# Kernel optimization log

Hardware: AMD Instinct MI355X
Metric: run time of the kernel (lower is better)

Reference implementation:

```python
import jax, jax.numpy as jnp
import numpy as np
import math

# ---- static config (matches init_kwargs) ----
N_USERS = 40000
N_ITEMS = 30000
N_ENTITIES = 80000
N_REL = 8            # edge_type in [1, N_REL), relation_emb has N_REL-1 rows
DIM = 64
N_HEADS = 2
D_K = DIM // N_HEADS
N_HOPS = 2
E_KG = 800000
E_UI = 600000


def setup_inputs() -> dict:
    key = jax.random.key(0)
    ks = jax.random.split(key, 10)
    return {
        "user_emb": jax.random.normal(ks[0], (N_USERS, DIM), jnp.float32) * 0.1,
        "entity_emb": jax.random.normal(ks[1], (N_ENTITIES, DIM), jnp.float32) * 0.1,
        "relation_emb": jax.random.normal(ks[2], (N_REL - 1, DIM), jnp.float32) * 0.1,
        "W_Q": jax.random.normal(ks[3], (DIM, DIM), jnp.float32) * (1.0 / math.sqrt(DIM)),
        "inter_edge_w": jax.random.uniform(ks[4], (E_UI,), jnp.float32),
        "edge_head": jax.random.randint(ks[5], (E_KG,), 0, N_ENTITIES, jnp.int32),
        "edge_tail": jax.random.randint(ks[6], (E_KG,), 0, N_ENTITIES, jnp.int32),
        "edge_type": jax.random.randint(ks[7], (E_KG,), 1, N_REL, jnp.int32),
        "inter_user": jax.random.randint(ks[8], (E_UI,), 0, N_USERS, jnp.int32),
        "inter_item": jax.random.randint(ks[9], (E_UI,), 0, N_ENTITIES, jnp.int32),
    }


def _seg_softmax(x, seg, n):
    """Numerically-stable softmax over edges grouped by segment id (scatter_softmax)."""
    m = jax.ops.segment_max(x, seg, num_segments=n)
    m = jnp.where(jnp.isneginf(m), 0.0, m)          # empty segments
    ex = jnp.exp(x - m[seg])
    s = jax.ops.segment_sum(ex, seg, num_segments=n)
    return ex / (s[seg] + 1e-16)


def _edge_attn(entity_emb, relation_emb, W_Q, head, tail, etype):
    """Per-edge multi-head attention logits: q_h . (k_h * rel_h) / sqrt(d_k). [E, H]"""
    q = (entity_emb[head] @ W_Q).reshape(-1, N_HEADS, D_K)
    k = (entity_emb[tail] @ W_Q).reshape(-1, N_HEADS, D_K)
    k = k * relation_emb[etype - 1].reshape(-1, N_HEADS, D_K)
    return (q * k).sum(-1) * (1.0 / math.sqrt(D_K))


def _l2norm(x):
    return x / jnp.maximum(jnp.linalg.norm(x, axis=-1, keepdims=True), 1e-12)


def reference(user_emb, entity_emb, relation_emb, W_Q, inter_edge_w,
              edge_head, edge_tail, edge_type, inter_user, inter_item):
    # ---- norm_attn_computer (logits detached in original torch code) ----
    logits = jax.lax.stop_gradient(
        _edge_attn(entity_emb, relation_emb, W_Q, edge_head, edge_tail, edge_type).mean(-1))  # [E]
    score = _seg_softmax(logits, edge_head, N_ENTITIES)
    deg = jax.ops.segment_sum(jnp.ones((E_KG,), jnp.float32), edge_head, num_segments=N_ENTITIES)
    edge_attn_score = score * deg[edge_head]                                   # [E]
    item_attn_sumed = (jax.ops.segment_sum(logits, edge_head, num_segments=N_ENTITIES)
                       + jax.ops.segment_sum(logits, edge_tail, num_segments=N_ENTITIES))[:N_ITEMS]

    # ---- HGT message passing hops (mess_dropout=False) ----
    e, u = entity_emb, user_emb
    e_res, u_res = entity_emb, user_emb
    for _ in range(N_HOPS):
        attn = _edge_attn(e, relation_emb, W_Q, edge_head, edge_tail, edge_type)  # [E, H]
        s = _seg_softmax(attn, edge_head, N_ENTITIES)                              # [E, H]
        neigh = (e[edge_tail] * relation_emb[edge_type - 1]).reshape(-1, N_HEADS, D_K) * s[..., None]
        e_agg = jax.ops.segment_sum(neigh.reshape(-1, DIM), edge_head, num_segments=N_ENTITIES)
        # bipartite user<->item aggregation with interaction weights
        u_agg = jax.ops.segment_sum(inter_edge_w[:, None] * e[inter_item], inter_user,
                                    num_segments=N_USERS)
        e_agg = e_agg + jax.ops.segment_sum(inter_edge_w[:, None] * u[inter_user], inter_item,
                                            num_segments=N_ENTITIES)
        e, u = _l2norm(e_agg), _l2norm(u_agg)
        e_res, u_res = e_res + e, u_res + u

    node_res_emb = jnp.concatenate([u_res, e_res], axis=0)   # [N_USERS+N_ENTITIES, DIM]
    return node_res_emb, edge_attn_score, item_attn_sumed
```

## Files before the change

kernel.cpp:

```cpp
#include <hip/hip_runtime.h>
#include <math.h>

#define NUSERS 40000
#define NENT   80000
#define NITEMS 30000
#define DIM    64
#define EKG    800000
#define EUI    600000
#define NTOT   (NENT + NUSERS + NENT)
#define UBASE  NENT
#define IBASE  (NENT + NUSERS)

struct __align__(8) us4 { unsigned short x, y, z, w; };
static __device__ __forceinline__ float b2f(unsigned short b) {
    return __uint_as_float(((unsigned)b) << 16);
}
static __device__ __forceinline__ unsigned short f2b(float f) {
    unsigned u = __float_as_uint(f);
    return (unsigned short)((u + 0x7FFFu + ((u >> 16) & 1u)) >> 16);
}
static __device__ __forceinline__ float4 us4tof(us4 v) {
    return make_float4(b2f(v.x), b2f(v.y), b2f(v.z), b2f(v.w));
}
static __device__ __forceinline__ float4 ld4b(const unsigned short* p) {
    return us4tof(*(const us4*)p);
}
static __device__ __forceinline__ void st4b(unsigned short* p, float a, float b, float c, float d) {
    us4 v = {f2b(a), f2b(b), f2b(c), f2b(d)};
    *(us4*)p = v;
}

static __device__ __forceinline__ float grp16_sum(float v) {
    v += __shfl_xor(v, 1);
    v += __shfl_xor(v, 2);
    v += __shfl_xor(v, 4);
    v += __shfl_xor(v, 8);
    return v;
}

__global__ void count_kernel(const int* __restrict__ ehead, const int* __restrict__ etail,
                             const int* __restrict__ etype,
                             const int* __restrict__ iuser, const int* __restrict__ iitem,
                             const float* __restrict__ user_emb,
                             int* __restrict__ cnt,
                             int* __restrict__ hrK, int* __restrict__ hrU, int* __restrict__ hrI,
                             int* __restrict__ tpack, unsigned short* __restrict__ u0b) {
    int e = blockIdx.x * blockDim.x + threadIdx.x;
    if (e < EKG) {
        int h = __builtin_nontemporal_load(&ehead[e]);
        int r = atomicAdd(&cnt[h], 1);
        hrK[e] = (h << 15) | r;
        tpack[e] = __builtin_nontemporal_load(&etail[e]) |
                   ((__builtin_nontemporal_load(&etype[e]) - 1) << 20);
    }
    if (e < EUI) {
        int u = __builtin_nontemporal_load(&iuser[e]);
        int r = atomicAdd(&cnt[UBASE + u], 1);
        hrU[e] = (u << 16) | r;
        int it = __builtin_nontemporal_load(&iitem[e]);
        int r2 = atomicAdd(&cnt[IBASE + it], 1);
        hrI[e] = (it << 15) | r2;
    }
    if (e < NUSERS * (DIM / 4)) {
        float4 vv = *(const float4*)(user_emb + (size_t)e * 4);
        st4b(u0b + (size_t)e * 4, vv.x, vv.y, vv.z, vv.w);
    }
}

#define SCHUNK 2048
#define SBLOCKS ((NTOT + SCHUNK - 1) / SCHUNK)

__global__ void scanA_kernel(const int* __restrict__ cnt, int* __restrict__ bsum) {
    int b = blockIdx.x, tid = threadIdx.x;
    int base = b * SCHUNK + tid * 8;
    int ts = 0;
#pragma unroll
    for (int k = 0; k < 8; k++) {
        int i = base + k;
        ts += (i < NTOT) ? cnt[i] : 0;
    }
#pragma unroll
    for (int d = 1; d < 64; d <<= 1) ts += __shfl_xor(ts, d);
    __shared__ int ws[4];
    if ((tid & 63) == 0) ws[tid >> 6] = ts;
    __syncthreads();
    if (tid == 0) bsum[b] = ws[0] + ws[1] + ws[2] + ws[3];
}

__global__ void scanB_kernel(const int* __restrict__ bsum, int* __restrict__ bpre,
                             int* __restrict__ off) {
    int lane = threadIdx.x;
    int carry = 0;
    for (int base = 0; base < SBLOCKS; base += 64) {
        int i = base + lane;
        int x = (i < SBLOCKS) ? bsum[i] : 0;
        int inc = x;
#pragma unroll
        for (int d = 1; d < 64; d <<= 1) {
            int t = __shfl_up(inc, d);
            if (lane >= d) inc += t;
        }
        if (i < SBLOCKS) bpre[i] = carry + inc - x;
        carry += __shfl(inc, 63);
    }
    if (lane == 0) off[NTOT] = carry;
}

__global__ void scanC_kernel(const int* __restrict__ cnt, const int* __restrict__ bpre,
                             int* __restrict__ off) {
    __shared__ int wtot[4];
    int b = blockIdx.x, tid = threadIdx.x, lane = tid & 63, wid = tid >> 6;
    int base = b * SCHUNK + tid * 8;
    int vals[8];
    int ts = 0;
#pragma unroll
    for (int k = 0; k < 8; k++) {
        int i = base + k;
        int x = (i < NTOT) ? cnt[i] : 0;
        vals[k] = ts;
        ts += x;
    }
    int inc = ts;
#pragma unroll
    for (int d = 1; d < 64; d <<= 1) {
        int t = __shfl_up(inc, d);
        if (lane >= d) inc += t;
    }
    if (lane == 63) wtot[wid] = inc;
    __syncthreads();
    int wbase = 0;
    for (int w = 0; w < wid; w++) wbase += wtot[w];
    int tbase = bpre[b] + wbase + (inc - ts);
#pragma unroll
    for (int k = 0; k < 8; k++) {
        int i = base + k;
        if (i < NTOT) off[i] = tbase + vals[k];
    }
}

__global__ void fillKG_kernel(const int* __restrict__ hrK, const int* __restrict__ tpack,
                              const int* __restrict__ off,
                              int2* __restrict__ kgp, int lo, int hi) {
    int e = blockIdx.x * blockDim.x + threadIdx.x;
    if (e >= EKG) return;
    int v = __builtin_nontemporal_load(&hrK[e]);
    int h = ((unsigned)v) >> 15;
    if (h < (unsigned)lo || h >= (unsigned)hi) return;
    int p = off[h] + (v & 0x7FFF);
    kgp[p] = make_int2(__builtin_nontemporal_load(&tpack[e]), e);
}

__global__ void fillUIu_kernel(const int* __restrict__ hrU, const int* __restrict__ iitem,
                               const float* __restrict__ iwin, const int* __restrict__ off,
                               int2* __restrict__ upack, int lo, int hi) {
    int e = blockIdx.x * blockDim.x + threadIdx.x;
    if (e >= EUI) return;
    int v = __builtin_nontemporal_load(&hrU[e]);
    int u = ((unsigned)v) >> 16;
    if (u < (unsigned)lo || u >= (unsigned)hi) return;
    int p = off[UBASE + u] - EKG + (v & 0xFFFF);
    upack[p] = make_int2(__builtin_nontemporal_load(&iitem[e]),
                         __float_as_int(__builtin_nontemporal_load(&iwin[e])));
}

__global__ void fillUIi_kernel(const int* __restrict__ hrI, const int* __restrict__ iuser,
                               const float* __restrict__ iwin, const int* __restrict__ off,
                               int2* __restrict__ ipack, int lo, int hi) {
    int e = blockIdx.x * blockDim.x + threadIdx.x;
    if (e >= EUI) return;
    int v = __builtin_nontemporal_load(&hrI[e]);
    int it = ((unsigned)v) >> 15;
    if (it < (unsigned)lo || it >= (unsigned)hi) return;
    int p = off[IBASE + it] - (EKG + EUI) + (v & 0x7FFF);
    ipack[p] = make_int2(__builtin_nontemporal_load(&iuser[e]),
                         __float_as_int(__builtin_nontemporal_load(&iwin[e])));
}

template <int MODE>
__global__ void gemm_wq_kernel(const float* __restrict__ Xf,
                               unsigned short* __restrict__ T,
                               const float* __restrict__ W,
                               float* __restrict__ item_sum) {
    __shared__ float Wl[64 * 64];
    int tid = threadIdx.x;
    for (int i = tid; i < 64 * 64; i += 256) Wl[i] = W[i];
    __syncthreads();
    int rloc = tid >> 4;
    int c4 = (tid & 15) * 4;
    int row = blockIdx.x * 16 + rloc;
    float ax = 0, ay = 0, az = 0, aw = 0;
#pragma unroll 8
    for (int d = 0; d < 64; d++) {
        float xv = (MODE == 0) ? Xf[(size_t)row * DIM + d] : b2f(T[(size_t)row * 128 + 64 + d]);
        const float4 w = *(const float4*)&Wl[d * 64 + c4];
        ax += xv * w.x;
        ay += xv * w.y;
        az += xv * w.z;
        aw += xv * w.w;
    }
    st4b(T + (size_t)row * 128 + c4, ax, ay, az, aw);
    if (MODE == 0) {
        const float4 xx = *(const float4*)(Xf + (size_t)row * DIM + c4);
        st4b(T + (size_t)row * 128 + 64 + c4, xx.x, xx.y, xx.z, xx.w);
        int gid = blockIdx.x * 256 + tid;
        if (gid < NITEMS) item_sum[gid] = 0.f;
    }
}

template <bool HOP0>
__global__ void hop_kernel(const unsigned short* __restrict__ T,
                           const unsigned short* __restrict__ ub,
                           const float* __restrict__ rel,
                           const int* __restrict__ off,
                           const int2* __restrict__ kgp,
                           const int2* __restrict__ upack, const int2* __restrict__ ipack,
                           const float* __restrict__ ebase, const float* __restrict__ ubase,
                           float* __restrict__ e_res, float* __restrict__ u_res,
                           unsigned short* __restrict__ Tnxt, unsigned short* __restrict__ unxt,
                           float* __restrict__ logit, float* __restrict__ edge_score,
                           float* __restrict__ item_sum) {
    __shared__ float srel[7 * DIM];
    int tid = threadIdx.x;
    for (int i = tid; i < 7 * DIM; i += 256) srel[i] = rel[i];
    __syncthreads();
    int g = tid >> 4, l = tid & 15;
    int v = blockIdx.x * 16 + g;
    const float sc = 0.17677669529663687f;
    float ax = 0, ay = 0, az = 0, aw = 0;

    if (v < NENT) {
        int o0 = off[v], o1 = off[v + 1];
        int deg = o1 - o0;
        const float4 q = ld4b(T + (size_t)v * 128 + l * 4);
        float s_h = 0.f, s_lm = 0.f, lsum = 0.f;

        auto edge_compute = [&](unsigned t, int jj, float4 k, float4 ev) {
            int r = t >> 20;
            const float4 rv = *(const float4*)(srel + r * DIM + l * 4);
            float part = q.x * k.x * rv.x + q.y * k.y * rv.y + q.z * k.z * rv.z + q.w * k.w * rv.w;
            part += __shfl_xor(part, 1);
            part += __shfl_xor(part, 2);
            part += __shfl_xor(part, 4);
            part *= sc;
            float wgt = __expf(part);
            s_h += wgt;
            ax += wgt * ev.x * rv.x;
            ay += wgt * ev.y * rv.y;
            az += wgt * ev.z * rv.z;
            aw += wgt * ev.w * rv.w;
            if (HOP0) {
                float other = __shfl_xor(part, 8);
                float lm = 0.5f * (part + other);
                s_lm += __expf(lm);
                lsum += lm;
                if (l == 0) {
                    logit[jj] = lm;
                    int tail = t & 0xFFFFF;
                    if (tail < NITEMS) atomicAdd(&item_sum[tail], lm);
                }
            }
        };

        int j = o0;
        for (; j + 2 <= o1; j += 2) {
            int2 kp0 = kgp[j], kp1 = kgp[j + 1];
            const unsigned short* b0 = T + (size_t)((unsigned)kp0.x & 0xFFFFF) * 128 + l * 4;
            const unsigned short* b1 = T + (size_t)((unsigned)kp1.x & 0xFFFFF) * 128 + l * 4;
            us4 rk0 = *(const us4*)b0;
            us4 re0 = *(const us4*)(b0 + 64);
            us4 rk1 = *(const us4*)b1;
            us4 re1 = *(const us4*)(b1 + 64);
            edge_compute((unsigned)kp0.x, j, us4tof(rk0), us4tof(re0));
            edge_compute((unsigned)kp1.x, j + 1, us4tof(rk1), us4tof(re1));
        }
        if (j < o1) {
            int2 kp0 = kgp[j];
            const unsigned short* b0 = T + (size_t)((unsigned)kp0.x & 0xFFFFF) * 128 + l * 4;
            edge_compute((unsigned)kp0.x, j, ld4b(b0), ld4b(b0 + 64));
        }
        float inv_sh = 1.0f / (s_h + 1e-16f);
        ax *= inv_sh;
        ay *= inv_sh;
        az *= inv_sh;
        aw *= inv_sh;
        if (HOP0) {
            if (l == 0 && deg > 0 && v < NITEMS) atomicAdd(&item_sum[v], lsum);
            float inv_slm = 1.0f / (s_lm + 1e-16f);
            float degf = (float)deg;
            for (int jj = o0 + l; jj < o1; jj += 16)
                edge_score[kgp[jj].y] = __expf(logit[jj]) * inv_slm * degf;
        }
        int p0 = off[IBASE + v] - (EKG + EUI);
        int p1 = off[IBASE + v + 1] - (EKG + EUI);
        int j2 = p0;
        for (; j2 + 2 <= p1; j2 += 2) {
            int2 a = ipack[j2], b = ipack[j2 + 1];
            us4 ra = *(const us4*)(ub + (size_t)a.x * 64 + l * 4);
            us4 rb = *(const us4*)(ub + (size_t)b.x * 64 + l * 4);
            float wa = __int_as_float(a.y), wb = __int_as_float(b.y);
            float4 fa = us4tof(ra), fb = us4tof(rb);
            ax += wa * fa.x + wb * fb.x;
            ay += wa * fa.y + wb * fb.y;
            az += wa * fa.z + wb * fb.z;
            aw += wa * fa.w + wb * fb.w;
        }
        if (j2 < p1) {
            int2 a = ipack[j2];
            float wa = __int_as_float(a.y);
            float4 fa = ld4b(ub + (size_t)a.x * 64 + l * 4);
            ax += wa * fa.x;
            ay += wa * fa.y;
            az += wa * fa.z;
            aw += wa * fa.w;
        }
        float nsq = grp16_sum(ax * ax + ay * ay + az * az + aw * aw);
        float invn = 1.0f / fmaxf(sqrtf(nsq), 1e-12f);
        float ox = ax * invn, oy = ay * invn, oz = az * invn, ow = aw * invn;
        if (HOP0) {
            st4b(Tnxt + (size_t)v * 128 + 64 + l * 4, ox, oy, oz, ow);
        } else {
            size_t base = (size_t)v * DIM + l * 4;
            const float4 b0v = *(const float4*)(ebase + base);
            const float4 pv = ld4b(T + (size_t)v * 128 + 64 + l * 4);
            float4 ro = {b0v.x + pv.x + ox, b0v.y + pv.y + oy, b0v.z + pv.z + oz,
                         b0v.w + pv.w + ow};
            *(float4*)(e_res + base) = ro;
        }
    } else {
        int u = v - NENT;
        int p0 = off[UBASE + u] - EKG;
        int p1 = off[UBASE + u + 1] - EKG;
        int j2 = p0;
        for (; j2 + 2 <= p1; j2 += 2) {
            int2 a = upack[j2], b = upack[j2 + 1];
            us4 ra = *(const us4*)(T + (size_t)a.x * 128 + 64 + l * 4);
            us4 rb = *(const us4*)(T + (size_t)b.x * 128 + 64 + l * 4);
            float wa = __int_as_float(a.y), wb = __int_as_float(b.y);
            float4 fa = us4tof(ra), fb = us4tof(rb);
            ax += wa * fa.x + wb * fb.x;
            ay += wa * fa.y + wb * fb.y;
            az += wa * fa.z + wb * fb.z;
            aw += wa * fa.w + wb * fb.w;
        }
        if (j2 < p1) {
            int2 a = upack[j2];
            float wa = __int_as_float(a.y);
            float4 fa = ld4b(T + (size_t)a.x * 128 + 64 + l * 4);
            ax += wa * fa.x;
            ay += wa * fa.y;
            az += wa * fa.z;
            aw += wa * fa.w;
        }
        float nsq = grp16_sum(ax * ax + ay * ay + az * az + aw * aw);
        float invn = 1.0f / fmaxf(sqrtf(nsq), 1e-12f);
        float ox = ax * invn, oy = ay * invn, oz = az * invn, ow = aw * invn;
        if (HOP0) {
            st4b(unxt + (size_t)u * DIM + l * 4, ox, oy, oz, ow);
        } else {
            size_t base = (size_t)u * DIM + l * 4;
            const float4 b0v = *(const float4*)(ubase + base);
            const float4 pv = ld4b(ub + base);
            float4 ro = {b0v.x + pv.x + ox, b0v.y + pv.y + oy, b0v.z + pv.z + oz,
                         b0v.w + pv.w + ow};
            *(float4*)(u_res + base) = ro;
        }
    }
}

extern "C" void kernel_launch(void* const* d_in, const int* in_sizes, int n_in,
                              void* d_out, int out_size, void* d_ws, size_t ws_size,
                              hipStream_t stream) {
    const float* user_emb   = (const float*)d_in[0];
    const float* entity_emb = (const float*)d_in[1];
    const float* rel        = (const float*)d_in[2];
    const float* W_Q        = (const float*)d_in[3];
    const float* iwin       = (const float*)d_in[4];
    const int* ehead        = (const int*)d_in[5];
    const int* etail        = (const int*)d_in[6];
    const int* etype        = (const int*)d_in[7];
    const int* iuser        = (const int*)d_in[8];
    const int* iitem        = (const int*)d_in[9];

    float* out        = (float*)d_out;
    float* u_res      = out;
    float* e_res      = out + (size_t)NUSERS * DIM;
    float* edge_score = out + (size_t)(NUSERS + NENT) * DIM;
    float* item_sum   = edge_score + EKG;

    char* w = (char*)d_ws;
    auto alloc = [&](size_t bytes) -> void* {
        void* p = (void*)w;
        w += (bytes + 255) & ~(size_t)255;
        return p;
    };
    unsigned short* T0  = (unsigned short*)alloc((size_t)NENT * 128 * 2);
    unsigned short* T1  = (unsigned short*)alloc((size_t)NENT * 128 * 2);
    unsigned short* u0b = (unsigned short*)alloc((size_t)NUSERS * DIM * 2);
    unsigned short* uAb = (unsigned short*)alloc((size_t)NUSERS * DIM * 2);
    int2* kgp    = (int2*)alloc((size_t)EKG * 8);
    int2* upack  = (int2*)alloc((size_t)EUI * 8);
    int2* ipack  = (int2*)alloc((size_t)EUI * 8);
    int* hrK     = (int*)alloc((size_t)EKG * 4);
    int* hrU     = (int*)alloc((size_t)EUI * 4);
    int* hrI     = (int*)alloc((size_t)EUI * 4);
    int* tpack   = (int*)alloc((size_t)EKG * 4);
    float* logit = (float*)alloc((size_t)EKG * 4);
    int* cnt     = (int*)alloc((size_t)NTOT * 4);
    int* off     = (int*)alloc((size_t)(NTOT + 1) * 4);
    int* bsum    = (int*)alloc((size_t)SBLOCKS * 4);
    int* bpre    = (int*)alloc((size_t)SBLOCKS * 4);
    (void)ws_size; (void)in_sizes; (void)n_in; (void)out_size;

    hipMemsetAsync(cnt, 0, (size_t)NTOT * 4, stream);

    count_kernel<<<(EKG + 255) / 256, 256, 0, stream>>>(ehead, etail, etype, iuser, iitem,
                                                        user_emb, cnt, hrK, hrU, hrI, tpack, u0b);
    scanA_kernel<<<SBLOCKS, 256, 0, stream>>>(cnt, bsum);
    scanB_kernel<<<1, 64, 0, stream>>>(bsum, bpre, off);
    scanC_kernel<<<SBLOCKS, 256, 0, stream>>>(cnt, bpre, off);

    const int KGG = (EKG + 255) / 256, UIG = (EUI + 255) / 256;
    for (int p = 0; p < 2; p++)
        fillKG_kernel<<<KGG, 256, 0, stream>>>(hrK, tpack, off, kgp,
                                               p * 40000, (p + 1) * 40000);
    for (int p = 0; p < 2; p++)
        fillUIu_kernel<<<UIG, 256, 0, stream>>>(hrU, iitem, iwin, off, upack,
                                                p * 20000, (p + 1) * 20000);
    for (int p = 0; p < 2; p++)
        fillUIi_kernel<<<UIG, 256, 0, stream>>>(hrI, iuser, iwin, off, ipack,
                                                p * 40000, (p + 1) * 40000);

    const int HOPG = (NENT + NUSERS) / 16;

    gemm_wq_kernel<0><<<NENT / 16, 256, 0, stream>>>(entity_emb, T0, W_Q, item_sum);
    hop_kernel<true><<<HOPG, 256, 0, stream>>>(T0, u0b, rel, off, kgp, upack, ipack,
                                               nullptr, nullptr, nullptr, nullptr,
                                               T1, uAb, logit, edge_score, item_sum);

    gemm_wq_kernel<1><<<NENT / 16, 256, 0, stream>>>(nullptr, T1, W_Q, nullptr);
    hop_kernel<false><<<HOPG, 256, 0, stream>>>(T1, uAb, rel, off, kgp, upack, ipack,
                                                entity_emb, user_emb, e_res, u_res,
                                                nullptr, nullptr, nullptr, nullptr, nullptr);
}
```

Baseline: 326.7 us.

## Pad degree counters, unroll KG edge loop by four, add nontemporal loads/stores

Degree counters are spaced 16 ints apart so concurrent atomics from different nodes land on separate 64-byte lines, which should reduce atomic contention in the count kernel. The cost is a 16x larger memset and strided reads in the scan kernels. The KG edge loop is unrolled from two to four edges to raise memory-level parallelism. Streaming CSR reads in hop 1 and the UI loops, plus the edge_score scatter, now use nontemporal loads/stores to limit cache pollution.

Result: slower. 373.8 us (+14.4%).

```diff
diff --git a/kernel.cpp b/kernel.cpp
--- a/kernel.cpp
+++ b/kernel.cpp
@@ -10,6 +10,7 @@
 #define NTOT   (NENT + NUSERS + NENT)
 #define UBASE  NENT
 #define IBASE  (NENT + NUSERS)
+#define CPAD   16
 
 struct __align__(8) us4 { unsigned short x, y, z, w; };
 static __device__ __forceinline__ float b2f(unsigned short b) {
@@ -28,6 +29,13 @@
 static __device__ __forceinline__ void st4b(unsigned short* p, float a, float b, float c, float d) {
     us4 v = {f2b(a), f2b(b), f2b(c), f2b(d)};
     *(us4*)p = v;
+}
+static __device__ __forceinline__ int2 ldnt_i2(const int2* p) {
+    long long v = __builtin_nontemporal_load((const long long*)p);
+    int2 r;
+    r.x = (int)(v & 0xFFFFFFFFll);
+    r.y = (int)(((unsigned long long)v) >> 32);
+    return r;
 }
 
 static __device__ __forceinline__ float grp16_sum(float v) {
@@ -48,17 +56,17 @@
     int e = blockIdx.x * blockDim.x + threadIdx.x;
     if (e < EKG) {
         int h = __builtin_nontemporal_load(&ehead[e]);
-        int r = atomicAdd(&cnt[h], 1);
+        int r = atomicAdd(&cnt[(size_t)h * CPAD], 1);
         hrK[e] = (h << 15) | r;
         tpack[e] = __builtin_nontemporal_load(&etail[e]) |
                    ((__builtin_nontemporal_load(&etype[e]) - 1) << 20);
     }
     if (e < EUI) {
         int u = __builtin_nontemporal_load(&iuser[e]);
-        int r = atomicAdd(&cnt[UBASE + u], 1);
+        int r = atomicAdd(&cnt[(size_t)(UBASE + u) * CPAD], 1);
         hrU[e] = (u << 16) | r;
         int it = __builtin_nontemporal_load(&iitem[e]);
-        int r2 = atomicAdd(&cnt[IBASE + it], 1);
+        int r2 = atomicAdd(&cnt[(size_t)(IBASE + it) * CPAD], 1);
         hrI[e] = (it << 15) | r2;
     }
     if (e < NUSERS * (DIM / 4)) {
@@ -77,7 +85,7 @@
 #pragma unroll
     for (int k = 0; k < 8; k++) {
         int i = base + k;
-        ts += (i < NTOT) ? cnt[i] : 0;
+        ts += (i < NTOT) ? cnt[(size_t)i * CPAD] : 0;
     }
 #pragma unroll
     for (int d = 1; d < 64; d <<= 1) ts += __shfl_xor(ts, d);
@@ -116,7 +124,7 @@
 #pragma unroll
     for (int k = 0; k < 8; k++) {
         int i = base + k;
-        int x = (i < NTOT) ? cnt[i] : 0;
+        int x = (i < NTOT) ? cnt[(size_t)i * CPAD] : 0;
         vals[k] = ts;
         ts += x;
     }
@@ -262,18 +270,32 @@
         };
 
         int j = o0;
-        for (; j + 2 <= o1; j += 2) {
-            int2 kp0 = kgp[j], kp1 = kgp[j + 1];
+        for (; j + 4 <= o1; j += 4) {
+            int2 kp0, kp1, kp2, kp3;
+            if (HOP0) {
+                kp0 = kgp[j]; kp1 = kgp[j + 1]; kp2 = kgp[j + 2]; kp3 = kgp[j + 3];
+            } else {
+                kp0 = ldnt_i2(&kgp[j]); kp1 = ldnt_i2(&kgp[j + 1]);
+                kp2 = ldnt_i2(&kgp[j + 2]); kp3 = ldnt_i2(&kgp[j + 3]);
+            }
             const unsigned short* b0 = T + (size_t)((unsigned)kp0.x & 0xFFFFF) * 128 + l * 4;
             const unsigned short* b1 = T + (size_t)((unsigned)kp1.x & 0xFFFFF) * 128 + l * 4;
+            const unsigned short* b2 = T + (size_t)((unsigned)kp2.x & 0xFFFFF) * 128 + l * 4;
+            const unsigned short* b3 = T + (size_t)((unsigned)kp3.x & 0xFFFFF) * 128 + l * 4;
             us4 rk0 = *(const us4*)b0;
             us4 re0 = *(const us4*)(b0 + 64);
             us4 rk1 = *(const us4*)b1;
             us4 re1 = *(const us4*)(b1 + 64);
+            us4 rk2 = *(const us4*)b2;
+            us4 re2 = *(const us4*)(b2 + 64);
+            us4 rk3 = *(const us4*)b3;
+            us4 re3 = *(const us4*)(b3 + 64);
             edge_compute((unsigned)kp0.x, j, us4tof(rk0), us4tof(re0));
             edge_compute((unsigned)kp1.x, j + 1, us4tof(rk1), us4tof(re1));
-        }
-        if (j < o1) {
+            edge_compute((unsigned)kp2.x, j + 2, us4tof(rk2), us4tof(re2));
+            edge_compute((unsigned)kp3.x, j + 3, us4tof(rk3), us4tof(re3));
+        }
+        for (; j < o1; ++j) {
             int2 kp0 = kgp[j];
             const unsigned short* b0 = T + (size_t)((unsigned)kp0.x & 0xFFFFF) * 128 + l * 4;
             edge_compute((unsigned)kp0.x, j, ld4b(b0), ld4b(b0 + 64));
@@ -287,14 +309,16 @@
             if (l == 0 && deg > 0 && v < NITEMS) atomicAdd(&item_sum[v], lsum);
             float inv_slm = 1.0f / (s_lm + 1e-16f);
             float degf = (float)deg;
-            for (int jj = o0 + l; jj < o1; jj += 16)
-                edge_score[kgp[jj].y] = __expf(logit[jj]) * inv_slm * degf;
+            for (int jj = o0 + l; jj < o1; jj += 16) {
+                float es = __expf(logit[jj]) * inv_slm * degf;
+                __builtin_nontemporal_store(es, &edge_score[kgp[jj].y]);
+            }
         }
         int p0 = off[IBASE + v] - (EKG + EUI);
         int p1 = off[IBASE + v + 1] - (EKG + EUI);
         int j2 = p0;
         for (; j2 + 2 <= p1; j2 += 2) {
-            int2 a = ipack[j2], b = ipack[j2 + 1];
+            int2 a = ldnt_i2(&ipack[j2]), b = ldnt_i2(&ipack[j2 + 1]);
             us4 ra = *(const us4*)(ub + (size_t)a.x * 64 + l * 4);
             us4 rb = *(const us4*)(ub + (size_t)b.x * 64 + l * 4);
             float wa = __int_as_float(a.y), wb = __int_as_float(b.y);
@@ -332,7 +356,7 @@
         int p1 = off[UBASE + u + 1] - EKG;
         int j2 = p0;
         for (; j2 + 2 <= p1; j2 += 2) {
-            int2 a = upack[j2], b = upack[j2 + 1];
+            int2 a = ldnt_i2(&upack[j2]), b = ldnt_i2(&upack[j2 + 1]);
             us4 ra = *(const us4*)(T + (size_t)a.x * 128 + 64 + l * 4);
             us4 rb = *(const us4*)(T + (size_t)b.x * 128 + 64 + l * 4);
             float wa = __int_as_float(a.y), wb = __int_as_float(b.y);
@@ -405,13 +429,13 @@
     int* hrI     = (int*)alloc((size_t)EUI * 4);
     int* tpack   = (int*)alloc((size_t)EKG * 4);
     float* logit = (float*)alloc((size_t)EKG * 4);
-    int* cnt     = (int*)alloc((size_t)NTOT * 4);
+    int* cnt     = (int*)alloc((size_t)NTOT * CPAD * 4);
     int* off     = (int*)alloc((size_t)(NTOT + 1) * 4);
     int* bsum    = (int*)alloc((size_t)SBLOCKS * 4);
     int* bpre    = (int*)alloc((size_t)SBLOCKS * 4);
     (void)ws_size; (void)in_sizes; (void)n_in; (void)out_size;
 
-    hipMemsetAsync(cnt, 0, (size_t)NTOT * 4, stream);
+    hipMemsetAsync(cnt, 0, (size_t)NTOT * CPAD * 4, stream);
 
     count_kernel<<<(EKG + 255) / 256, 256, 0, stream>>>(ehead, etail, etype, iuser, iitem,
                                                         user_emb, cnt, hrK, hrU, hrI, tpack, u0b);
```

## Bucket nodes by degree for hop load balance and fuse first GEMM into count

Applied to the files above, without the earlier changes.

Adds a counting-sort pass (permA/B/C) that orders nodes by total degree, capped at 255, and the hop kernels map each 16-lane group to a node through this permutation. Nodes of similar degree then share a wavefront, which cuts divergence and tail imbalance. The hop-0 W_Q GEMM is also merged into the edge-counting kernel as extra blocks, removing one launch and letting the two independent jobs overlap. The cost is three small extra kernels, indirect node indexing that scatters row accesses, and a larger combined kernel that reserves 16KB of shared memory even in its counting blocks.

Result: slower. 577.6 us (+76.8%).

```diff
diff --git a/kernel.cpp b/kernel.cpp
--- a/kernel.cpp
+++ b/kernel.cpp
@@ -10,6 +10,9 @@
 #define NTOT   (NENT + NUSERS + NENT)
 #define UBASE  NENT
 #define IBASE  (NENT + NUSERS)
+#define NNODE  (NENT + NUSERS)
+#define BPAD   16
+#define GEMMB  (NENT / 16)
 
 struct __align__(8) us4 { unsigned short x, y, z, w; };
 static __device__ __forceinline__ float b2f(unsigned short b) {
@@ -38,32 +41,62 @@
     return v;
 }
 
-__global__ void count_kernel(const int* __restrict__ ehead, const int* __restrict__ etail,
-                             const int* __restrict__ etype,
-                             const int* __restrict__ iuser, const int* __restrict__ iitem,
-                             const float* __restrict__ user_emb,
-                             int* __restrict__ cnt,
-                             int* __restrict__ hrK, int* __restrict__ hrU, int* __restrict__ hrI,
-                             int* __restrict__ tpack, unsigned short* __restrict__ u0b) {
-    int e = blockIdx.x * blockDim.x + threadIdx.x;
-    if (e < EKG) {
-        int h = __builtin_nontemporal_load(&ehead[e]);
-        int r = atomicAdd(&cnt[h], 1);
-        hrK[e] = (h << 15) | r;
-        tpack[e] = __builtin_nontemporal_load(&etail[e]) |
-                   ((__builtin_nontemporal_load(&etype[e]) - 1) << 20);
-    }
-    if (e < EUI) {
-        int u = __builtin_nontemporal_load(&iuser[e]);
-        int r = atomicAdd(&cnt[UBASE + u], 1);
-        hrU[e] = (u << 16) | r;
-        int it = __builtin_nontemporal_load(&iitem[e]);
-        int r2 = atomicAdd(&cnt[IBASE + it], 1);
-        hrI[e] = (it << 15) | r2;
-    }
-    if (e < NUSERS * (DIM / 4)) {
-        float4 vv = *(const float4*)(user_emb + (size_t)e * 4);
-        st4b(u0b + (size_t)e * 4, vv.x, vv.y, vv.z, vv.w);
+__global__ void count_gemm_kernel(const float* __restrict__ Xf, unsigned short* __restrict__ T,
+                                  const float* __restrict__ W, float* __restrict__ item_sum,
+                                  const int* __restrict__ ehead, const int* __restrict__ etail,
+                                  const int* __restrict__ etype,
+                                  const int* __restrict__ iuser, const int* __restrict__ iitem,
+                                  const float* __restrict__ user_emb,
+                                  int* __restrict__ cnt,
+                                  int* __restrict__ hrK, int* __restrict__ hrU,
+                                  int* __restrict__ hrI,
+                                  int* __restrict__ tpack, unsigned short* __restrict__ u0b,
+                                  int* __restrict__ bcnt) {
+    int tid = threadIdx.x;
+    if (blockIdx.x < GEMMB) {
+        __shared__ float Wl[64 * 64];
+        for (int i = tid; i < 64 * 64; i += 256) Wl[i] = W[i];
+        __syncthreads();
+        int rloc = tid >> 4;
+        int c4 = (tid & 15) * 4;
+        int row = blockIdx.x * 16 + rloc;
+        float ax = 0, ay = 0, az = 0, aw = 0;
+#pragma unroll 8
+        for (int d = 0; d < 64; d++) {
+            float xv = Xf[(size_t)row * DIM + d];
+            const float4 w = *(const float4*)&Wl[d * 64 + c4];
+            ax += xv * w.x;
+            ay += xv * w.y;
+            az += xv * w.z;
+            aw += xv * w.w;
+        }
+        st4b(T + (size_t)row * 128 + c4, ax, ay, az, aw);
+        const float4 xx = *(const float4*)(Xf + (size_t)row * DIM + c4);
+        st4b(T + (size_t)row * 128 + 64 + c4, xx.x, xx.y, xx.z, xx.w);
+        int gid = blockIdx.x * 256 + tid;
+        if (gid < NITEMS) item_sum[gid] = 0.f;
+        if (blockIdx.x == 0) bcnt[tid * BPAD] = 0;
+    } else {
+        int e = (blockIdx.x - GEMMB) * 256 + tid;
+        if (e < EKG) {
+            int h = __builtin_nontemporal_load(&ehead[e]);
+            int r = atomicAdd(&cnt[h], 1);
+            hrK[e] = (h << 15) | r;
+            tpack[e] = __builtin_nontemporal_load(&etail[e]) |
+                       ((__builtin_nontemporal_load(&etype[e]) - 1) << 20);
+        }
+        if (e < EUI) {
+            int u = __builtin_nontemporal_load(&iuser[e]);
+            int r = atomicAdd(&cnt[UBASE + u], 1);
+            hrU[e] = (u << 16) | r;
+            int it = __builtin_nontemporal_load(&iitem[e]);
+            int r2 = atomicAdd(&cnt[IBASE + it], 1);
+            hrI[e] = (it << 15) | r2;
+        }
+        if (e < NUSERS * (DIM / 4)) {
+            float4 vv = *(const float4*)(user_emb + (size_t)e * 4);
+            st4b(u0b + (size_t)e * 4, vv.x, vv.y, vv.z, vv.w);
+        }
     }
 }
 
@@ -136,6 +169,44 @@
         int i = base + k;
         if (i < NTOT) off[i] = tbase + vals[k];
     }
+}
+
+__global__ void permA_kernel(const int* __restrict__ cnt, int* __restrict__ bcnt,
+                             int* __restrict__ pb) {
+    int v = blockIdx.x * 256 + threadIdx.x;
+    if (v >= NNODE) return;
+    int wk = (v < NENT) ? (cnt[v] + cnt[IBASE + v]) : cnt[UBASE + (v - NENT)];
+    int b = min(wk, 255);
+    int r = atomicAdd(&bcnt[b * BPAD], 1);
+    pb[v] = (r << 8) | b;
+}
+
+__global__ void permB_kernel(const int* __restrict__ bcnt, int* __restrict__ bpre2) {
+    int lane = threadIdx.x & 63;
+    int loc[4];
+    int s = 0;
+#pragma unroll
+    for (int k = 0; k < 4; k++) {
+        loc[k] = s;
+        s += bcnt[(lane * 4 + k) * BPAD];
+    }
+    int inc = s;
+#pragma unroll
+    for (int d = 1; d < 64; d <<= 1) {
+        int t = __shfl_up(inc, d);
+        if (lane >= d) inc += t;
+    }
+    int excl = inc - s;
+#pragma unroll
+    for (int k = 0; k < 4; k++) bpre2[lane * 4 + k] = excl + loc[k];
+}
+
+__global__ void permC_kernel(const int* __restrict__ pb, const int* __restrict__ bpre2,
+                             int* __restrict__ perm) {
+    int v = blockIdx.x * 256 + threadIdx.x;
+    if (v >= NNODE) return;
+    int x = pb[v];
+    perm[bpre2[x & 255] + (((unsigned)x) >> 8)] = v;
 }
 
 __global__ void fillKG_kernel(const int* __restrict__ hrK, const int* __restrict__ tpack,
@@ -176,11 +247,7 @@
                          __float_as_int(__builtin_nontemporal_load(&iwin[e])));
 }
 
-template <int MODE>
-__global__ void gemm_wq_kernel(const float* __restrict__ Xf,
-                               unsigned short* __restrict__ T,
-                               const float* __restrict__ W,
-                               float* __restrict__ item_sum) {
+__global__ void gemm1_kernel(unsigned short* __restrict__ T, const float* __restrict__ W) {
     __shared__ float Wl[64 * 64];
     int tid = threadIdx.x;
     for (int i = tid; i < 64 * 64; i += 256) Wl[i] = W[i];
@@ -191,7 +258,7 @@
     float ax = 0, ay = 0, az = 0, aw = 0;
 #pragma unroll 8
     for (int d = 0; d < 64; d++) {
-        float xv = (MODE == 0) ? Xf[(size_t)row * DIM + d] : b2f(T[(size_t)row * 128 + 64 + d]);
+        float xv = b2f(T[(size_t)row * 128 + 64 + d]);
         const float4 w = *(const float4*)&Wl[d * 64 + c4];
         ax += xv * w.x;
         ay += xv * w.y;
@@ -199,16 +266,11 @@
         aw += xv * w.w;
     }
     st4b(T + (size_t)row * 128 + c4, ax, ay, az, aw);
-    if (MODE == 0) {
-        const float4 xx = *(const float4*)(Xf + (size_t)row * DIM + c4);
-        st4b(T + (size_t)row * 128 + 64 + c4, xx.x, xx.y, xx.z, xx.w);
-        int gid = blockIdx.x * 256 + tid;
-        if (gid < NITEMS) item_sum[gid] = 0.f;
-    }
 }
 
 template <bool HOP0>
-__global__ void hop_kernel(const unsigned short* __restrict__ T,
+__global__ void hop_kernel(const int* __restrict__ perm,
+                           const unsigned short* __restrict__ T,
                            const unsigned short* __restrict__ ub,
                            const float* __restrict__ rel,
                            const int* __restrict__ off,
@@ -224,7 +286,7 @@
     for (int i = tid; i < 7 * DIM; i += 256) srel[i] = rel[i];
     __syncthreads();
     int g = tid >> 4, l = tid & 15;
-    int v = blockIdx.x * 16 + g;
+    int v = perm[blockIdx.x * 16 + g];
     const float sc = 0.17677669529663687f;
     float ax = 0, ay = 0, az = 0, aw = 0;
 
@@ -407,17 +469,27 @@
     float* logit = (float*)alloc((size_t)EKG * 4);
     int* cnt     = (int*)alloc((size_t)NTOT * 4);
     int* off     = (int*)alloc((size_t)(NTOT + 1) * 4);
-    int* bsum    = (int*)alloc((size_t)SBLOCKS * 4);
-    int* bpre    = (int*)alloc((size_t)SBLOCKS * 4);
+    int* sbsum   = (int*)alloc((size_t)SBLOCKS * 4);
+    int* sbpre   = (int*)alloc((size_t)SBLOCKS * 4);
+    int* bcnt    = (int*)alloc((size_t)256 * BPAD * 4);
+    int* bpre2   = (int*)alloc((size_t)256 * 4);
+    int* pb      = (int*)alloc((size_t)NNODE * 4);
+    int* perm    = (int*)alloc((size_t)NNODE * 4);
     (void)ws_size; (void)in_sizes; (void)n_in; (void)out_size;
 
     hipMemsetAsync(cnt, 0, (size_t)NTOT * 4, stream);
 
-    count_kernel<<<(EKG + 255) / 256, 256, 0, stream>>>(ehead, etail, etype, iuser, iitem,
-                                                        user_emb, cnt, hrK, hrU, hrI, tpack, u0b);
-    scanA_kernel<<<SBLOCKS, 256, 0, stream>>>(cnt, bsum);
-    scanB_kernel<<<1, 64, 0, stream>>>(bsum, bpre, off);
-    scanC_kernel<<<SBLOCKS, 256, 0, stream>>>(cnt, bpre, off);
+    count_gemm_kernel<<<GEMMB + (EKG + 255) / 256, 256, 0, stream>>>(
+        entity_emb, T0, W_Q, item_sum, ehead, etail, etype, iuser, iitem, user_emb,
+        cnt, hrK, hrU, hrI, tpack, u0b, bcnt);
+
+    scanA_kernel<<<SBLOCKS, 256, 0, stream>>>(cnt, sbsum);
+    scanB_kernel<<<1, 64, 0, stream>>>(sbsum, sbpre, off);
+    scanC_kernel<<<SBLOCKS, 256, 0, stream>>>(cnt, sbpre, off);
+
+    permA_kernel<<<(NNODE + 255) / 256, 256, 0, stream>>>(cnt, bcnt, pb);
+    permB_kernel<<<1, 64, 0, stream>>>(bcnt, bpre2);
+    permC_kernel<<<(NNODE + 255) / 256, 256, 0, stream>>>(pb, bpre2, perm);
 
     const int KGG = (EKG + 255) / 256, UIG = (EUI + 255) / 256;
     for (int p = 0; p < 2; p++)
@@ -430,15 +502,14 @@
         fillUIi_kernel<<<UIG, 256, 0, stream>>>(hrI, iuser, iwin, off, ipack,
                                                 p * 40000, (p + 1) * 40000);
 
-    const int HOPG = (NENT + NUSERS) / 16;
-
-    gemm_wq_kernel<0><<<NENT / 16, 256, 0, stream>>>(entity_emb, T0, W_Q, item_sum);
-    hop_kernel<true><<<HOPG, 256, 0, stream>>>(T0, u0b, rel, off, kgp, upack, ipack,
+    const int HOPG = NNODE / 16;
+
+    hop_kernel<true><<<HOPG, 256, 0, stream>>>(perm, T0, u0b, rel, off, kgp, upack, ipack,
                                                nullptr, nullptr, nullptr, nullptr,
                                                T1, uAb, logit, edge_score, item_sum);
 
-    gemm_wq_kernel<1><<<NENT / 16, 256, 0, stream>>>(nullptr, T1, W_Q, nullptr);
-    hop_kernel<false><<<HOPG, 256, 0, stream>>>(T1, uAb, rel, off, kgp, upack, ipack,
+    gemm1_kernel<<<NENT / 16, 256, 0, stream>>>(T1, W_Q);
+    hop_kernel<false><<<HOPG, 256, 0, stream>>>(perm, T1, uAb, rel, off, kgp, upack, ipack,
                                                 entity_emb, user_emb, e_res, u_res,
                                                 nullptr, nullptr, nullptr, nullptr, nullptr);
 }
```
